# Performance work log

Measured on AMD Instinct MI355X. Metric: run time of the kernel, lower is better.

Reference implementation:

```python
import jax, jax.numpy as jnp
import numpy as np

N_QUBITS = 8


def _cnot_perm(n, c, t):
    idx = np.arange(2 ** n)
    cbit = (idx >> (n - 1 - c)) & 1
    return np.where(cbit == 1, idx ^ (1 << (n - 1 - t)), idx)

CNOT_PERMS = [jnp.asarray(_cnot_perm(N_QUBITS, q, (q + 1) % N_QUBITS)) for q in range(N_QUBITS)]


def _apply_1q(state, q, U):
    # state: (N, 2^n) complex; U: (2,2) shared or (N,2,2) per-token
    N = state.shape[0]
    s = state.reshape(N, 2 ** q, 2, -1)
    if U.ndim == 2:
        s = jnp.einsum('ab,nibj->niaj', U, s)
    else:
        s = jnp.einsum('nab,nibj->niaj', U, s)
    return s.reshape(N, -1)


def _ry(theta):
    c, s = jnp.cos(theta / 2), jnp.sin(theta / 2)
    return jnp.stack([jnp.stack([c, -s], -1), jnp.stack([s, c], -1)], -2).astype(jnp.complex64)


def _rz(theta):
    e = jnp.exp(0.5j * theta.astype(jnp.complex64))
    z = jnp.zeros_like(e)
    return jnp.stack([jnp.stack([jnp.conj(e), z], -1), jnp.stack([z, e], -1)], -2)


def _quantum_states(x, theta):
    # x: (N, n_qubits) encoding angles; theta: (L, n_qubits, 2)
    N, n = x.shape
    state = jnp.zeros((N, 2 ** n), jnp.complex64).at[:, 0].set(1.0)
    for q in range(n):  # RY angle encoding
        state = _apply_1q(state, q, _ry(x[:, q]))
    for l in range(theta.shape[0]):  # variational layers
        for q in range(n):
            state = _apply_1q(state, q, _ry(theta[l, q, 0]))
            state = _apply_1q(state, q, _rz(theta[l, q, 1]))
        for q in range(n):  # ring entangler CNOT(q, q+1)
            state = state[:, CNOT_PERMS[q]]
    return state


def setup_inputs() -> dict:
    key = jax.random.key(0)
    ks = jax.random.split(key, 8)
    B, S, E, n, L = 128, 128, 1024, N_QUBITS, 4
    return {
        'X': jax.random.normal(ks[0], (B, S, E), jnp.float32),
        'Wi': jax.random.normal(ks[1], (E, n), jnp.float32) * 0.02,
        'bi': jnp.zeros((n,), jnp.float32),
        'Wv': jax.random.normal(ks[2], (E, E), jnp.float32) * 0.02,
        'bv': jnp.zeros((E,), jnp.float32),
        'Wo': jax.random.normal(ks[3], (E, E), jnp.float32) * 0.02,
        'bo': jnp.zeros((E,), jnp.float32),
        'theta': jax.random.normal(ks[4], (L, n, 2), jnp.float32) * 0.1,
        'phi': jax.random.normal(ks[5], (S,), jnp.float32) * 0.1,
    }


def reference(X, Wi, bi, Wv, bv, Wo, bo, theta, phi):
    B, S, E = X.shape
    qin = X @ Wi + bi          # (B,S,n_qubits)
    V = X @ Wv + bv            # (B,S,E)
    psi = _quantum_states(qin.reshape(B * S, -1), theta).reshape(B, S, -1)
    G = jnp.einsum('bsd,btd->bst', psi, jnp.conj(psi))  # overlaps
    K = (G.real ** 2 + G.imag ** 2) / jnp.sqrt(jnp.float32(N_QUBITS))
    phi_s = phi[:S]
    K = K + jnp.cos(phi_s[None, :] - phi_s[:, None])    # cosine positional bias
    attn = jax.nn.softmax(K, axis=-1)                   # (B,S,S)
    out = jnp.einsum('bst,bte->bse', attn, V)
    y = out @ Wo + bo
    return y, attn
```

## Files before the change

kernel.cpp:

```cpp
#include <hip/hip_runtime.h>
#include <hip/hip_bf16.h>

#define BB 128
#define SS 128
#define EE 1024
#define NQ 8
#define DD 256
#define LL 4
#define MM (BB*SS)

typedef unsigned short bf16s;
typedef __attribute__((ext_vector_type(8))) short bf16x8;
typedef __attribute__((ext_vector_type(4))) float f32x4;

#define AS1 __attribute__((address_space(1)))
#define AS3 __attribute__((address_space(3)))

__device__ __forceinline__ unsigned short f2bf(float x) {
    unsigned u = __float_as_uint(x);
    u += 0x7fffu + ((u >> 16) & 1u);
    return (unsigned short)(u >> 16);
}

#define PIPE_WAIT(N) do { \
    asm volatile("s_waitcnt vmcnt(" #N ")" ::: "memory"); \
    __builtin_amdgcn_sched_barrier(0); \
    __builtin_amdgcn_s_barrier(); \
    __builtin_amdgcn_sched_barrier(0); } while (0)
#define PIPE_BAR() do { \
    __builtin_amdgcn_sched_barrier(0); \
    __builtin_amdgcn_s_barrier(); } while (0)

__global__ __launch_bounds__(256) void transpose_conv_kernel(
    const float* __restrict__ in, bf16s* __restrict__ out, int R, int C)
{
    __shared__ float t[32][33];
    int bx = blockIdx.x * 32, by = blockIdx.y * 32;
    int lx = threadIdx.x & 31, ly = threadIdx.x >> 5;
#pragma unroll
    for (int i = 0; i < 32; i += 8)
        t[ly + i][lx] = in[(size_t)(by + ly + i) * C + bx + lx];
    __syncthreads();
#pragma unroll
    for (int i = 0; i < 32; i += 8)
        out[(size_t)(bx + ly + i) * R + by + lx] = f2bf(t[lx][ly + i]);
}

__global__ __launch_bounds__(256) void cvt_kernel(
    const float* __restrict__ in, bf16s* __restrict__ out)
{
    int g = blockIdx.x * 256 + threadIdx.x;
    f32x4 x = ((const f32x4*)in)[g];
    ushort4 o;
    o.x = f2bf(x[0]); o.y = f2bf(x[1]); o.z = f2bf(x[2]); o.w = f2bf(x[3]);
    ((ushort4*)out)[g] = o;
}

__global__ __launch_bounds__(256) void bvo_part_kernel(
    const float* __restrict__ bv, const float* __restrict__ Wo,
    float* __restrict__ part)
{
    __shared__ float red[4][64];
    int lane = threadIdx.x & 63, w = threadIdx.x >> 6;
    int eb = blockIdx.x & 15, kb = blockIdx.x >> 4;
    int e = eb * 64 + lane;
    int k0 = kb * 64 + w * 16;
    float acc = 0.f;
#pragma unroll
    for (int i = 0; i < 16; i++)
        acc += bv[k0 + i] * Wo[(size_t)(k0 + i) * EE + e];
    red[w][lane] = acc;
    __syncthreads();
    if (w == 0)
        part[kb * EE + e] = red[0][lane] + red[1][lane] + red[2][lane] + red[3][lane];
}

__global__ __launch_bounds__(256) void bvo_reduce_kernel(
    const float* __restrict__ part, const float* __restrict__ bo,
    float* __restrict__ bvo)
{
    int e = blockIdx.x * 256 + threadIdx.x;
    float s = bo[e];
#pragma unroll
    for (int kb = 0; kb < 16; kb++) s += part[kb * EE + e];
    bvo[e] = s;
}

__global__ __launch_bounds__(256) void wtrans_kernel(
    const float* __restrict__ Wi, float* __restrict__ Wit)
{
    int g = blockIdx.x * 256 + threadIdx.x;
    int k = g >> 3, j = g & 7;
    Wit[j * 1024 + k] = Wi[g];
}

__global__ __launch_bounds__(256) void encode_kernel(
    const float* __restrict__ X, const float* __restrict__ Wit,
    const float* __restrict__ bi,
    bf16s* __restrict__ Xb, bf16s* __restrict__ v)
{
    const int lane = threadIdx.x & 63;
    const int wid  = threadIdx.x >> 6;
    const int row  = blockIdx.x * 4 + wid;

    const f32x4* xr4 = (const f32x4*)(X + (size_t)row * EE);
    ushort4* xbr4 = (ushort4*)(Xb + (size_t)row * EE);

    float acc[NQ];
#pragma unroll
    for (int j = 0; j < NQ; j++) acc[j] = 0.f;

#pragma unroll
    for (int t = 0; t < 4; t++) {
        int k4 = t * 64 + lane;
        f32x4 x = xr4[k4];
        ushort4 xb;
        xb.x = f2bf(x[0]); xb.y = f2bf(x[1]);
        xb.z = f2bf(x[2]); xb.w = f2bf(x[3]);
        xbr4[k4] = xb;
#pragma unroll
        for (int j = 0; j < NQ; j++) {
            f32x4 w = ((const f32x4*)(Wit + j * 1024))[k4];
            acc[j] += x[0]*w[0] + x[1]*w[1] + x[2]*w[2] + x[3]*w[3];
        }
    }
    float qin[NQ];
#pragma unroll
    for (int j = 0; j < NQ; j++) {
        float s = acc[j];
#pragma unroll
        for (int off = 32; off >= 1; off >>= 1) s += __shfl_xor(s, off, 64);
        qin[j] = s + bi[j];
    }

    float cs[NQ], sn[NQ];
#pragma unroll
    for (int q = 0; q < NQ; q++) __sincosf(0.5f * qin[q], &sn[q], &cs[q]);

    float common = 1.f;
#pragma unroll
    for (int b = 2; b < 8; b++) {
        int q = 7 - b;
        common *= ((lane >> (b - 2)) & 1) ? sn[q] : cs[q];
    }
    float a0 = common * cs[6] * cs[7];
    float a1 = common * cs[6] * sn[7];
    float a2 = common * sn[6] * cs[7];
    float a3 = common * sn[6] * sn[7];
    ushort4 vo;
    vo.x = f2bf(a0); vo.y = f2bf(a1); vo.z = f2bf(a2); vo.w = f2bf(a3);
    ((ushort4*)(v + (size_t)row * DD))[lane] = vo;
}

template<bool OUT_BF16>
__global__ __launch_bounds__(256) void mfma_gemm(
    const bf16s* __restrict__ A, const bf16s* __restrict__ Bt,
    const float* __restrict__ bias, void* __restrict__ Cv,
    int M, int N, int K, int nm, int nn,
    long long sA, long long sB, long long sC)
{
    __shared__ bf16s As[3][128 * 32];
    __shared__ bf16s Bs[3][128 * 32];

    const int tid  = threadIdx.x;
    const int wave = tid >> 6, lane = tid & 63;
    const int quad = lane >> 4, lr = lane & 15;
    const int wm = (wave >> 1) * 64, wn = (wave & 1) * 64;

    const int nwg = gridDim.x;
    const int q = nwg >> 3, r = nwg & 7;
    const int xcd = blockIdx.x & 7, idx = blockIdx.x >> 3;
    const int w = (xcd < r ? xcd * (q + 1) : r * (q + 1) + (xcd - r) * q) + idx;
    const int n_t = w % nn;
    const int m_t = (w / nn) % nm;
    const int z   = w / (nn * nm);
    const int m0 = m_t * 128, n0 = n_t * 128;

    A  += (size_t)z * sA;
    Bt += (size_t)z * sB;

    f32x4 acc[4][4];
#pragma unroll
    for (int i = 0; i < 4; i++)
#pragma unroll
        for (int j = 0; j < 4; j++) acc[i][j] = (f32x4){0.f, 0.f, 0.f, 0.f};

    auto stage = [&](int buf, int kt) {
#pragma unroll
        for (int j = 0; j < 2; j++) {
            int ch = j * 256 + tid;
            int row = ch >> 2, kc = (ch & 3) * 8;
            __builtin_amdgcn_global_load_lds(
                (AS1 const void*)(A + (size_t)(m0 + row) * K + kt + kc),
                (AS3 void*)(As[buf] + (size_t)(j * 256 + wave * 64) * 8), 16, 0, 0);
            __builtin_amdgcn_global_load_lds(
                (AS1 const void*)(Bt + (size_t)(n0 + row) * K + kt + kc),
                (AS3 void*)(Bs[buf] + (size_t)(j * 256 + wave * 64) * 8), 16, 0, 0);
        }
    };
    auto compute = [&](int buf) {
        bf16x8 af[4], bfr[4];
#pragma unroll
        for (int i = 0; i < 4; i++)
            af[i] = *(const bf16x8*)(As[buf] + (wm + i * 16 + lr) * 32 + quad * 8);
#pragma unroll
        for (int j = 0; j < 4; j++)
            bfr[j] = *(const bf16x8*)(Bs[buf] + (wn + j * 16 + lr) * 32 + quad * 8);
#pragma unroll
        for (int i = 0; i < 4; i++)
#pragma unroll
            for (int j = 0; j < 4; j++)
                acc[i][j] = __builtin_amdgcn_mfma_f32_16x16x32_bf16(
                    af[i], bfr[j], acc[i][j], 0, 0, 0);
    };

    const int nt = K >> 5;
    stage(0, 0);
    stage(1, 1 << 5);
    int cur = 0, nxt = 2;
    for (int t = 0; t < nt; t++) {
        if (t + 2 < nt) { stage(nxt, (t + 2) << 5); PIPE_WAIT(8); }
        else if (t + 1 < nt) PIPE_WAIT(4);
        else PIPE_WAIT(0);
        compute(cur);
        PIPE_BAR();
        cur = (cur == 2) ? 0 : cur + 1;
        nxt = (nxt == 2) ? 0 : nxt + 1;
    }

    float* Cf = (float*)Cv + (size_t)z * sC;
    bf16s* Cb = (bf16s*)Cv + (size_t)z * sC;
#pragma unroll
    for (int i = 0; i < 4; i++) {
        int row0 = m0 + wm + i * 16 + quad * 4;
#pragma unroll
        for (int j = 0; j < 4; j++) {
            int col = n0 + wn + j * 16 + lr;
            float bb = bias ? bias[col] : 0.f;
#pragma unroll
            for (int r = 0; r < 4; r++) {
                float v = acc[i][j][r] + bb;
                if (OUT_BF16) Cb[(size_t)(row0 + r) * N + col] = f2bf(v);
                else          Cf[(size_t)(row0 + r) * N + col] = v;
            }
        }
    }
}

__global__ __launch_bounds__(256) void attn_kernel(
    const bf16s* __restrict__ v, const float* __restrict__ phi,
    float* __restrict__ attn, bf16s* __restrict__ attn_bf)
{
    __shared__ bf16s Bs[3][128 * 32];

    const int tid  = threadIdx.x;
    const int wave = tid >> 6, lane = tid & 63;
    const int quad = lane >> 4, lr = lane & 15;
    const int b = blockIdx.y;
    const int s0 = blockIdx.x * 64;
    const bf16s* vb = v + (size_t)b * 128 * DD;

    f32x4 accre[8];
#pragma unroll
    for (int j = 0; j < 8; j++) accre[j] = (f32x4){0.f, 0.f, 0.f, 0.f};

    auto stage = [&](int buf, int kt) {
#pragma unroll
        for (int j = 0; j < 2; j++) {
            int ch = j * 256 + tid;
            int row = ch >> 2, kc = (ch & 3) * 8;
            __builtin_amdgcn_global_load_lds(
                (AS1 const void*)(vb + (size_t)row * DD + kt + kc),
                (AS3 void*)(Bs[buf] + (size_t)(j * 256 + wave * 64) * 8), 16, 0, 0);
        }
    };
    auto compute = [&](int buf) {
        bf16x8 afr = *(const bf16x8*)(Bs[buf] + (s0 + wave * 16 + lr) * 32 + quad * 8);
#pragma unroll
        for (int j = 0; j < 8; j++) {
            bf16x8 b1 = *(const bf16x8*)(Bs[buf] + (j * 16 + lr) * 32 + quad * 8);
            accre[j] = __builtin_amdgcn_mfma_f32_16x16x32_bf16(afr, b1, accre[j], 0, 0, 0);
        }
    };

    const int nt = DD >> 5;
    stage(0, 0);
    stage(1, 1 << 5);
    int cur = 0, nxt = 2;
    for (int t = 0; t < nt; t++) {
        if (t + 2 < nt) { stage(nxt, (t + 2) << 5); PIPE_WAIT(4); }
        else if (t + 1 < nt) PIPE_WAIT(2);
        else PIPE_WAIT(0);
        compute(cur);
        PIPE_BAR();
        cur = (cur == 2) ? 0 : cur + 1;
        nxt = (nxt == 2) ? 0 : nxt + 1;
    }

    const float isq = 0.35355339059327373f;
    float ph_r[4], ph_c[8];
#pragma unroll
    for (int r = 0; r < 4; r++) ph_r[r] = phi[s0 + wave * 16 + quad * 4 + r];
#pragma unroll
    for (int j = 0; j < 8; j++) ph_c[j] = phi[j * 16 + lr];

#pragma unroll
    for (int r = 0; r < 4; r++) {
        float vv[8];
        float mx = -1e30f;
#pragma unroll
        for (int j = 0; j < 8; j++) {
            float re = accre[j][r];
            vv[j] = re * re * isq + __cosf(ph_c[j] - ph_r[r]);
            mx = fmaxf(mx, vv[j]);
        }
#pragma unroll
        for (int off = 1; off <= 8; off <<= 1) mx = fmaxf(mx, __shfl_xor(mx, off, 64));
        float sm = 0.f;
#pragma unroll
        for (int j = 0; j < 8; j++) { vv[j] = __expf(vv[j] - mx); sm += vv[j]; }
#pragma unroll
        for (int off = 1; off <= 8; off <<= 1) sm += __shfl_xor(sm, off, 64);
        float inv = 1.f / sm;
        int srow = b * 128 + s0 + wave * 16 + quad * 4 + r;
#pragma unroll
        for (int j = 0; j < 8; j++) {
            float o = vv[j] * inv;
            attn[(size_t)srow * 128 + j * 16 + lr] = o;
            attn_bf[(size_t)srow * 128 + j * 16 + lr] = f2bf(o);
        }
    }
}

extern "C" void kernel_launch(void* const* d_in, const int* in_sizes, int n_in,
                              void* d_out, int out_size, void* d_ws, size_t ws_size,
                              hipStream_t stream) {
    const float* X     = (const float*)d_in[0];
    const float* Wi    = (const float*)d_in[1];
    const float* bi    = (const float*)d_in[2];
    const float* Wv    = (const float*)d_in[3];
    const float* bv    = (const float*)d_in[4];
    const float* Wo    = (const float*)d_in[5];
    const float* bo    = (const float*)d_in[6];
    const float* phi   = (const float*)d_in[8];

    float* y    = (float*)d_out;
    float* attn = y + (size_t)MM * EE;

    bf16s* Xb   = (bf16s*)d_ws;
    bf16s* Vwtb = Xb  + (size_t)MM * EE;
    bf16s* v    = Vwtb + (size_t)MM * EE;
    bf16s* abf  = v   + (size_t)MM * DD;
    bf16s* Wvb  = abf + (size_t)BB * SS * SS;
    bf16s* Wot  = Wvb + (size_t)EE * EE;
    bf16s* Wvot = Wot + (size_t)EE * EE;
    float* Wit  = (float*)(Wvot + (size_t)EE * EE);
    float* bvo  = Wit + 8 * 1024;
    float* bvop = bvo + 1024;

    wtrans_kernel<<<32, 256, 0, stream>>>(Wi, Wit);
    encode_kernel<<<MM / 4, 256, 0, stream>>>(X, Wit, bi, Xb, v);
    transpose_conv_kernel<<<dim3(32, 32), 256, 0, stream>>>(Wo, Wot, EE, EE);
    cvt_kernel<<<1024, 256, 0, stream>>>(Wv, Wvb);
    bvo_part_kernel<<<256, 256, 0, stream>>>(bv, Wo, bvop);
    bvo_reduce_kernel<<<4, 256, 0, stream>>>(bvop, bo, bvo);
    mfma_gemm<true><<<64, 256, 0, stream>>>(
        Wot, Wvb, nullptr, Wvot, EE, EE, EE, 8, 8, 0, 0, 0);
    attn_kernel<<<dim3(2, BB), 256, 0, stream>>>(v, phi, attn, abf);
    mfma_gemm<true><<<1024, 256, 0, stream>>>(
        Wvot, Xb, nullptr, Vwtb, EE, SS, EE, 8, 1,
        0, (long long)SS * EE, (long long)EE * SS);
    mfma_gemm<false><<<1024, 256, 0, stream>>>(
        abf, Vwtb, bvo, y, SS, EE, SS, 1, 8,
        (long long)SS * SS, (long long)EE * SS, (long long)SS * EE);
}
```

Before: 274.1 us.

## Replace batched V projection GEMM with single 256x256-tile GEMM over all tokens

The per-batch (Wvo × X_b^T) GEMM with 128x128 tiles is replaced by one large GEMM producing Vwt as E×(B·S), using 256x256 tiles, 512 threads, a 4-slot LDS pipeline and XOR-swizzled LDS layout to avoid bank conflicts. The final attention GEMM now reads Vwt with a leading dimension of B·S via a new ldB parameter and a batch stride of S. The aim is more operand reuse per tile and fewer, larger workgroups. In exchange it uses 128KB of dynamic LDS, which limits occupancy, and it depends on correct stride changes in the consumer GEMM.

```diff
diff --git a/kernel.cpp b/kernel.cpp
--- a/kernel.cpp
+++ b/kernel.cpp
@@ -152,11 +152,101 @@
     ((ushort4*)(v + (size_t)row * DD))[lane] = vo;
 }
 
+__global__ __launch_bounds__(512) void gemm256_kernel(
+    const bf16s* __restrict__ A, const bf16s* __restrict__ Bt,
+    bf16s* __restrict__ C, int M, int N, int K, int nm, int nn)
+{
+    extern __shared__ bf16s lds[];
+    bf16s* As = lds;
+    bf16s* Bs = lds + 4 * 8192;
+
+    const int tid  = threadIdx.x;
+    const int lane = tid & 63;
+    const int wid  = tid >> 6;
+    const int quad = lane >> 4, lr = lane & 15;
+    const int wr = wid >> 2, wc = wid & 3;
+
+    const int nwg = gridDim.x;
+    const int q = nwg >> 3, r = nwg & 7;
+    const int xcd = blockIdx.x & 7, idx = blockIdx.x >> 3;
+    const int w = (xcd < r ? xcd * (q + 1) : r * (q + 1) + (xcd - r) * q) + idx;
+    const int n_t = w % nn, m_t = w / nn;
+    const int m0 = m_t * 256, n0 = n_t * 256;
+
+    f32x4 acc[8][4];
+#pragma unroll
+    for (int i = 0; i < 8; i++)
+#pragma unroll
+        for (int j = 0; j < 4; j++) acc[i][j] = (f32x4){0.f, 0.f, 0.f, 0.f};
+
+    auto stage = [&](int slot, int kt) {
+#pragma unroll
+        for (int l = 0; l < 2; l++) {
+            int ch = l * 512 + tid;
+            int row = ch >> 2;
+            int kc = ((ch & 3) ^ (row & 3)) * 8;
+            __builtin_amdgcn_global_load_lds(
+                (AS1 const void*)(A + (size_t)(m0 + row) * K + kt * 32 + kc),
+                (AS3 void*)(As + slot * 8192 + ch * 8), 16, 0, 0);
+        }
+#pragma unroll
+        for (int l = 0; l < 2; l++) {
+            int ch = l * 512 + tid;
+            int row = ch >> 2;
+            int kc = ((ch & 3) ^ (row & 3)) * 8;
+            __builtin_amdgcn_global_load_lds(
+                (AS1 const void*)(Bt + (size_t)(n0 + row) * K + kt * 32 + kc),
+                (AS3 void*)(Bs + slot * 8192 + ch * 8), 16, 0, 0);
+        }
+    };
+    auto compute = [&](int slot) {
+        bf16x8 af[8];
+#pragma unroll
+        for (int i = 0; i < 8; i++) {
+            int rowl = wr * 128 + i * 16 + lr;
+            af[i] = *(const bf16x8*)(As + slot * 8192 + rowl * 32
+                                     + ((quad ^ (rowl & 3)) * 8));
+        }
+#pragma unroll
+        for (int j = 0; j < 4; j++) {
+            int rowl = wc * 64 + j * 16 + lr;
+            bf16x8 bfr = *(const bf16x8*)(Bs + slot * 8192 + rowl * 32
+                                          + ((quad ^ (rowl & 3)) * 8));
+#pragma unroll
+            for (int i = 0; i < 8; i++)
+                acc[i][j] = __builtin_amdgcn_mfma_f32_16x16x32_bf16(
+                    af[i], bfr, acc[i][j], 0, 0, 0);
+        }
+    };
+
+    const int NT = K >> 5;
+    stage(0, 0);
+    stage(1, 1);
+    for (int kt = 0; kt < NT; kt++) {
+        if (kt + 1 < NT) PIPE_WAIT(4);
+        else             PIPE_WAIT(0);
+        if (kt + 2 < NT) stage((kt + 2) & 3, kt + 2);
+        compute(kt & 3);
+    }
+
+#pragma unroll
+    for (int i = 0; i < 8; i++) {
+        int row0 = m0 + wr * 128 + i * 16 + quad * 4;
+#pragma unroll
+        for (int j = 0; j < 4; j++) {
+            int col = n0 + wc * 64 + j * 16 + lr;
+#pragma unroll
+            for (int rr = 0; rr < 4; rr++)
+                C[(size_t)(row0 + rr) * N + col] = f2bf(acc[i][j][rr]);
+        }
+    }
+}
+
 template<bool OUT_BF16>
 __global__ __launch_bounds__(256) void mfma_gemm(
     const bf16s* __restrict__ A, const bf16s* __restrict__ Bt,
     const float* __restrict__ bias, void* __restrict__ Cv,
-    int M, int N, int K, int nm, int nn,
+    int M, int N, int K, int ldB, int nm, int nn,
     long long sA, long long sB, long long sC)
 {
     __shared__ bf16s As[3][128 * 32];
@@ -194,7 +284,7 @@
                 (AS1 const void*)(A + (size_t)(m0 + row) * K + kt + kc),
                 (AS3 void*)(As[buf] + (size_t)(j * 256 + wave * 64) * 8), 16, 0, 0);
             __builtin_amdgcn_global_load_lds(
-                (AS1 const void*)(Bt + (size_t)(n0 + row) * K + kt + kc),
+                (AS1 const void*)(Bt + (size_t)(n0 + row) * ldB + kt + kc),
                 (AS3 void*)(Bs[buf] + (size_t)(j * 256 + wave * 64) * 8), 16, 0, 0);
         }
     };
@@ -348,8 +438,8 @@
     float* attn = y + (size_t)MM * EE;
 
     bf16s* Xb   = (bf16s*)d_ws;
-    bf16s* Vwtb = Xb  + (size_t)MM * EE;
-    bf16s* v    = Vwtb + (size_t)MM * EE;
+    bf16s* Vwt  = Xb  + (size_t)MM * EE;
+    bf16s* v    = Vwt + (size_t)MM * EE;
     bf16s* abf  = v   + (size_t)MM * DD;
     bf16s* Wvb  = abf + (size_t)BB * SS * SS;
     bf16s* Wot  = Wvb + (size_t)EE * EE;
@@ -365,12 +455,11 @@
     bvo_part_kernel<<<256, 256, 0, stream>>>(bv, Wo, bvop);
     bvo_reduce_kernel<<<4, 256, 0, stream>>>(bvop, bo, bvo);
     mfma_gemm<true><<<64, 256, 0, stream>>>(
-        Wot, Wvb, nullptr, Wvot, EE, EE, EE, 8, 8, 0, 0, 0);
+        Wot, Wvb, nullptr, Wvot, EE, EE, EE, EE, 8, 8, 0, 0, 0);
     attn_kernel<<<dim3(2, BB), 256, 0, stream>>>(v, phi, attn, abf);
-    mfma_gemm<true><<<1024, 256, 0, stream>>>(
-        Wvot, Xb, nullptr, Vwtb, EE, SS, EE, 8, 1,
-        0, (long long)SS * EE, (long long)EE * SS);
+    gemm256_kernel<<<256, 512, 128 * 1024, stream>>>(
+        Wvot, Xb, Vwt, EE, MM, EE, 4, 64);
     mfma_gemm<false><<<1024, 256, 0, stream>>>(
-        abf, Vwtb, bvo, y, SS, EE, SS, 1, 8,
-        (long long)SS * SS, (long long)EE * SS, (long long)SS * EE);
-}
+        abf, Vwt, bvo, y, SS, EE, SS, MM, 1, 8,
+        (long long)SS * SS, (long long)SS, (long long)SS * EE);
+}
```

Result: faster. 257.0 us (-6.2%).
